# Performance work log

Hardware: AMD Instinct MI355X
Metric: run time of the kernel (lower is better)

The kernel has to match this reference:

```python
import jax, jax.numpy as jnp
import numpy as np

SEGMENT_LENGTHS = (2048, 4096, 8192)
DILATION_RATES = (1, 2, 4)


def _attention(q, k, v):
    # q,k,v: (B, s, h, d); xformers default scale = 1/sqrt(d), no mask, no dropout
    d = q.shape[-1]
    scale = 1.0 / jnp.sqrt(jnp.asarray(d, q.dtype))
    scores = jnp.einsum('bshd,bthd->bhst', q, k) * scale
    p = jax.nn.softmax(scores, axis=-1)
    return jnp.einsum('bhst,bthd->bshd', p, v)


def setup_inputs() -> dict:
    key = jax.random.key(0)
    kq, kk, kv = jax.random.split(key, 3)
    shape = (2, 8192, 12, 64)
    return {
        'query': jax.random.normal(kq, shape, dtype=jnp.float32),
        'key': jax.random.normal(kk, shape, dtype=jnp.float32),
        'value': jax.random.normal(kv, shape, dtype=jnp.float32),
    }


def reference(query, key, value):
    b, n, h, d = query.shape
    num_groups = len(DILATION_RATES)
    group_sizes = [h // num_groups] * num_groups
    for i in range(h % num_groups):
        group_sizes[i] += 1
    out = jnp.zeros_like(query)
    for i, (g, r, s) in enumerate(zip(group_sizes, DILATION_RATES, SEGMENT_LENGTHS)):
        nseg = n // s
        offset = i % r
        hmin, hmax = i * g, (i + 1) * g
        # gather: segment, dilate (stride r), select head group
        qg = query.reshape(b, nseg, s, h, d)[:, :, offset::r, hmin:hmax, :]
        kg = key.reshape(b, nseg, s, h, d)[:, :, offset::r, hmin:hmax, :]
        vg = value.reshape(b, nseg, s, h, d)[:, :, offset::r, hmin:hmax, :]
        sd = qg.shape[2]  # dilated segment length
        x = _attention(
            qg.reshape(b * nseg, sd, g, d),
            kg.reshape(b * nseg, sd, g, d),
            vg.reshape(b * nseg, sd, g, d),
        ).reshape(b, nseg, sd, g, d)
        # normalization over (segments, dilated positions), as in the original
        x = x / x.sum(axis=(1, 2), keepdims=True)
        out_r = out.reshape(b, nseg, s, h, d)
        out_r = out_r.at[:, :, offset::r, hmin:hmax, :].add(x)
        out = out_r.reshape(b, n, h, d)
    return out / num_groups
```

## Files before the change

kernel.cpp:

```cpp
#include <hip/hip_runtime.h>
#include <math.h>

#define TOK_STRIDE 768

typedef __attribute__((ext_vector_type(8))) _Float16 f16x8;
typedef __attribute__((ext_vector_type(16))) float f32x16;

__device__ __forceinline__ int inst_index(int g, int b, int seg, int gh) {
    if (g == 0) return b * 16 + seg * 4 + gh;
    if (g == 1) return 32 + b * 8 + seg * 4 + gh;
    return 48 + b * 4 + gh;
}

__device__ __forceinline__ void decode_inst(int inst, int& g, int& b, int& seg, int& gh) {
    if (inst < 32)      { g = 0; int x = inst;      b = x >> 4; seg = (x >> 2) & 3; gh = x & 3; }
    else if (inst < 48) { g = 1; int x = inst - 32; b = x >> 3; seg = (x >> 2) & 1; gh = x & 3; }
    else                { g = 2; int x = inst - 48; b = x >> 2; seg = 0;            gh = x & 3; }
}

__device__ __forceinline__ long inst_base(int g, int b, int seg, int gh, long& tstep) {
    int r = 1 << g, s = 2048 << g, off = (g == 0) ? 0 : g, h = g * 4 + gh;
    tstep = (long)r * TOK_STRIDE;
    long tok0 = (long)seg * s + off;
    return ((long)b * 8192 + tok0) * TOK_STRIDE + (long)h * 64;
}

__device__ __forceinline__ void h_split(float x, unsigned short& hi, unsigned short& lo) {
    _Float16 h = (_Float16)x;
    _Float16 l = (_Float16)(x - (float)h);
    hi = __builtin_bit_cast(unsigned short, h);
    lo = __builtin_bit_cast(unsigned short, l);
}

__device__ __forceinline__ unsigned h2_rn(float a, float b) {
    unsigned short ua = __builtin_bit_cast(unsigned short, (_Float16)a);
    unsigned short ub = __builtin_bit_cast(unsigned short, (_Float16)b);
    return (unsigned)ua | ((unsigned)ub << 16);
}

__device__ __forceinline__ void gload_lds16(void* lds, const void* g) {
    __builtin_amdgcn_global_load_lds(
        (const __attribute__((address_space(1))) unsigned int*)g,
        (__attribute__((address_space(3))) unsigned int*)lds, 16, 0, 0);
}

__global__ __launch_bounds__(256) void prep_kernel(
    const float* __restrict__ K, const float* __restrict__ V,
    unsigned short* __restrict__ Kh, unsigned short* __restrict__ Kl,
    unsigned short* __restrict__ Vth, unsigned short* __restrict__ Vtl)
{
    const int kt = blockIdx.x, inst = blockIdx.y;
    int g, b, seg, gh; decode_inst(inst, g, b, seg, gh);
    long tstep; const long base = inst_base(g, b, seg, gh, tstep);
    const float* kb = K + base;
    const float* vb = V + base;
    const int t = threadIdx.x;

    __shared__ float Vs[64][72];

    #pragma unroll
    for (int p = 0; p < 4; ++p) {
        int flat = p * 256 + t;
        int key = flat >> 4;
        int d0 = (flat & 15) * 4;
        const long src = ((long)(kt * 64 + key)) * tstep + d0;
        float4 xk = *(const float4*)(kb + src);
        float kvals[4] = {xk.x, xk.y, xk.z, xk.w};
        unsigned short hi[4], lo[4];
        #pragma unroll
        for (int e = 0; e < 4; ++e) h_split(kvals[e], hi[e], lo[e]);
        int dc = d0 >> 4, hh = (d0 >> 3) & 1, j = d0 & 7;
        long idx = ((((long)inst * 32 + kt) * 8 + dc * 2 + hh) * 64 + key) * 8 + j;
        *(ushort4*)(Kh + idx) = make_ushort4(hi[0], hi[1], hi[2], hi[3]);
        *(ushort4*)(Kl + idx) = make_ushort4(lo[0], lo[1], lo[2], lo[3]);
        float4 xv = *(const float4*)(vb + src);
        float vvals[4] = {xv.x, xv.y, xv.z, xv.w};
        #pragma unroll
        for (int e = 0; e < 4; ++e) {
            int d = d0 + e;
            Vs[d][key ^ ((((d) >> 2) & 7) << 3)] = vvals[e];
        }
    }
    __syncthreads();
    #pragma unroll
    for (int p = 0; p < 4; ++p) {
        int flat = p * 256 + t;
        int d = flat >> 4;
        int k40 = (flat & 15) * 4;
        int swz = ((d >> 2) & 7) << 3;
        float4 xv = *(const float4*)&Vs[d][k40 ^ swz];
        float vvals[4] = {xv.x, xv.y, xv.z, xv.w};
        unsigned short hi[4], lo[4];
        #pragma unroll
        for (int e = 0; e < 4; ++e) h_split(vvals[e], hi[e], lo[e]);
        int k = kt * 64 + k40;
        int kc = k >> 4, hh = (k >> 3) & 1, j = k & 7;
        long idx = ((((long)inst * 128 + kc) * 2 + hh) * 64 + d) * 8 + j;
        *(ushort4*)(Vth + idx) = make_ushort4(hi[0], hi[1], hi[2], hi[3]);
        *(ushort4*)(Vtl + idx) = make_ushort4(lo[0], lo[1], lo[2], lo[3]);
    }
}

__global__ __launch_bounds__(256, 2) void attn_kernel(
    const float* __restrict__ Q,
    const unsigned short* __restrict__ Kh, const unsigned short* __restrict__ Kl,
    const unsigned short* __restrict__ Vth, const unsigned short* __restrict__ Vtl,
    float* __restrict__ O)
{
    const int rt = blockIdx.x, inst = blockIdx.y;
    int g, b, seg, gh; decode_inst(inst, g, b, seg, gh);
    long tstep; const long base = inst_base(g, b, seg, gh, tstep);
    const float* qb = Q + base;

    __shared__ unsigned short KVb[2][16384];
    __shared__ unsigned short Pb[4][2048];

    const int t = threadIdx.x;
    const int lane = t & 63;
    const int w = t >> 6;
    const int l31 = lane & 31;
    const int h = lane >> 5;

    const float* qp = qb + (long)(rt * 128 + w * 32 + l31) * tstep;
    f16x8 Qhf[4], Qlf[4];
    #pragma unroll
    for (int dc = 0; dc < 4; ++dc) {
        float4 f0 = *(const float4*)(qp + dc * 16 + h * 8);
        float4 f1 = *(const float4*)(qp + dc * 16 + h * 8 + 4);
        float vals[8] = {f0.x, f0.y, f0.z, f0.w, f1.x, f1.y, f1.z, f1.w};
        #pragma unroll
        for (int j = 0; j < 8; ++j) {
            float x = vals[j] * 0.125f;
            _Float16 hi = (_Float16)x;
            _Float16 lo = (_Float16)(x - (float)hi);
            Qhf[dc][j] = hi;
            Qlf[dc][j] = lo;
        }
    }

    const unsigned short* sbase = (w == 0) ? Kh : (w == 1) ? Kl : (w == 2) ? Vth : Vtl;
    const unsigned short* sp0 = sbase + (long)inst * 131072;
    #pragma unroll
    for (int i = 0; i < 8; ++i)
        gload_lds16(&KVb[0][w * 4096 + i * 512], sp0 + i * 512 + lane * 8);

    f32x16 o0, o1;
    #pragma unroll
    for (int rr = 0; rr < 16; ++rr) { o0[rr] = 0.f; o1[rr] = 0.f; }
    float m = -INFINITY, lsum = 0.f;

    __syncthreads();

    for (int kt = 0; kt < 32; ++kt) {
        const int cb = kt & 1;
        if (kt + 1 < 32) {
            const unsigned short* sp = sp0 + (long)(kt + 1) * 4096;
            #pragma unroll
            for (int i = 0; i < 8; ++i)
                gload_lds16(&KVb[cb ^ 1][w * 4096 + i * 512], sp + i * 512 + lane * 8);
        }

        f32x16 sS[2];
        #pragma unroll
        for (int a = 0; a < 2; ++a)
            #pragma unroll
            for (int rr = 0; rr < 16; ++rr) sS[a][rr] = 0.f;

        #pragma unroll
        for (int dc = 0; dc < 4; ++dc) {
            #pragma unroll
            for (int kt2 = 0; kt2 < 2; ++kt2) {
                int aoff = ((dc * 2 + h) * 64 + kt2 * 32 + l31) * 8;
                f16x8 kh = *(const f16x8*)&KVb[cb][aoff];
                f16x8 kl = *(const f16x8*)&KVb[cb][4096 + aoff];
                sS[kt2] = __builtin_amdgcn_mfma_f32_32x32x16_f16(kh, Qhf[dc], sS[kt2], 0, 0, 0);
                sS[kt2] = __builtin_amdgcn_mfma_f32_32x32x16_f16(kh, Qlf[dc], sS[kt2], 0, 0, 0);
                sS[kt2] = __builtin_amdgcn_mfma_f32_32x32x16_f16(kl, Qhf[dc], sS[kt2], 0, 0, 0);
            }
        }

        float pmax = -INFINITY;
        #pragma unroll
        for (int a = 0; a < 2; ++a)
            #pragma unroll
            for (int rr = 0; rr < 16; ++rr) pmax = fmaxf(pmax, sS[a][rr]);
        pmax = fmaxf(pmax, __shfl_xor(pmax, 32));

        if (!__all(pmax <= m + 8.f)) {
            float mnew = fmaxf(m, pmax);
            float f = __expf(m - mnew);
            m = mnew;
            lsum *= f;
            #pragma unroll
            for (int rr = 0; rr < 16; ++rr) { o0[rr] *= f; o1[rr] *= f; }
        }
        float psum = 0.f;
        #pragma unroll
        for (int a = 0; a < 2; ++a)
            #pragma unroll
            for (int rr = 0; rr < 16; ++rr) {
                float p = __expf(sS[a][rr] - m);
                sS[a][rr] = p;
                psum += p;
            }
        psum += __shfl_xor(psum, 32);
        lsum += psum;

        #pragma unroll
        for (int kt2 = 0; kt2 < 2; ++kt2) {
            #pragma unroll
            for (int qd = 0; qd < 4; ++qd) {
                unsigned w0 = h2_rn(sS[kt2][qd * 4 + 0], sS[kt2][qd * 4 + 1]);
                unsigned w1 = h2_rn(sS[kt2][qd * 4 + 2], sS[kt2][qd * 4 + 3]);
                int k = kt2 * 32 + qd * 8 + 4 * h;
                int kc = k >> 4, hh = (k >> 3) & 1, j = k & 7;
                int idx = ((kc * 2 + hh) * 32 + l31) * 8 + j;
                *(uint2*)&Pb[w][idx] = make_uint2(w0, w1);
            }
        }

        #pragma unroll
        for (int kc = 0; kc < 4; ++kc) {
            f16x8 pf = *(const f16x8*)&Pb[w][((kc * 2 + h) * 32 + l31) * 8];
            int voff = ((kc * 2 + h) * 64 + l31) * 8;
            f16x8 vh0 = *(const f16x8*)&KVb[cb][8192 + voff];
            f16x8 vl0 = *(const f16x8*)&KVb[cb][12288 + voff];
            f16x8 vh1 = *(const f16x8*)&KVb[cb][8192 + voff + 256];
            f16x8 vl1 = *(const f16x8*)&KVb[cb][12288 + voff + 256];
            o0 = __builtin_amdgcn_mfma_f32_32x32x16_f16(vh0, pf, o0, 0, 0, 0);
            o0 = __builtin_amdgcn_mfma_f32_32x32x16_f16(vl0, pf, o0, 0, 0, 0);
            o1 = __builtin_amdgcn_mfma_f32_32x32x16_f16(vh1, pf, o1, 0, 0, 0);
            o1 = __builtin_amdgcn_mfma_f32_32x32x16_f16(vl1, pf, o1, 0, 0, 0);
        }

        __syncthreads();
    }

    float inv = 1.0f / lsum;
    const int q = rt * 128 + w * 32 + l31;
    float* op = O + ((long)inst * 2048 + q) * 64;
    #pragma unroll
    for (int c = 0; c < 4; ++c) {
        int d0 = c * 8 + 4 * h;
        *(float4*)(op + d0) = make_float4(o0[c * 4] * inv, o0[c * 4 + 1] * inv,
                                          o0[c * 4 + 2] * inv, o0[c * 4 + 3] * inv);
        *(float4*)(op + 32 + d0) = make_float4(o1[c * 4] * inv, o1[c * 4 + 1] * inv,
                                               o1[c * 4 + 2] * inv, o1[c * 4 + 3] * inv);
    }
}

__global__ __launch_bounds__(256) void sum_kernel(
    const float* __restrict__ O, double* __restrict__ partial)
{
    const int blk = blockIdx.x;
    const int c   = blockIdx.y;
    const int g   = blk >> 3;
    const int b   = (blk >> 2) & 1;
    const int gh  = blk & 3;
    const int nseg = 4 >> g;
    const int R = nseg << 11;
    const int chunk = R >> 4;

    const int t  = threadIdx.x;
    const int d  = t & 63;
    const int rc = t >> 6;

    double acc = 0.0;
    for (int jr = c * chunk + rc; jr < (c + 1) * chunk; jr += 4) {
        int seg  = jr >> 11;
        int j    = jr & 2047;
        int inst = inst_index(g, b, seg, gh);
        acc += (double)O[(long)inst * 131072 + (long)j * 64 + d];
    }
    __shared__ double red[256];
    red[t] = acc;
    __syncthreads();
    if (rc == 0)
        partial[((long)blk * 16 + c) * 64 + d] =
            red[d] + red[64 + d] + red[128 + d] + red[192 + d];
}

__global__ void inv_kernel(const double* __restrict__ partial, double* __restrict__ invden)
{
    const int blk = blockIdx.x;
    const int d   = threadIdx.x;
    double s = 0.0;
    #pragma unroll
    for (int c = 0; c < 16; ++c) s += partial[((long)blk * 16 + c) * 64 + d];
    invden[blk * 64 + d] = 1.0 / (3.0 * s);
}

__global__ __launch_bounds__(256) void out_kernel(
    const float* __restrict__ O, const double* __restrict__ invden,
    float* __restrict__ out)
{
    const int f = blockIdx.x * 256 + threadIdx.x;
    const int d  = f & 63;
    const int hh = (f >> 6) % 12;
    const int tk = (f / 768) % 8192;
    const int b  = f / (768 * 8192);

    const int g  = hh >> 2;
    const int gh = hh & 3;
    const int r  = 1 << g;
    const int off = (g == 0) ? 0 : g;

    const int seg = tk >> (11 + g);
    const int pos = tk - (seg << (11 + g));
    const int rem = pos - off;

    float val = 0.f;
    if (rem >= 0 && (rem & (r - 1)) == 0) {
        const int j = rem >> g;
        const int inst = inst_index(g, b, seg, gh);
        float num = O[(long)inst * 131072 + (long)j * 64 + d];
        double iv = invden[(long)(g * 8 + b * 4 + gh) * 64 + d];
        val = (float)((double)num * iv);
    }
    out[f] = val;
}

extern "C" void kernel_launch(void* const* d_in, const int* in_sizes, int n_in,
                              void* d_out, int out_size, void* d_ws, size_t ws_size,
                              hipStream_t stream) {
    const float* q = (const float*)d_in[0];
    const float* k = (const float*)d_in[1];
    const float* v = (const float*)d_in[2];
    float* out = (float*)d_out;

    char* ws = (char*)d_ws;
    double* invden  = (double*)(ws);
    double* partial = (double*)(ws + 12288);
    float*  Ows     = (float*)(ws + 208896);
    unsigned short* Khp  = (unsigned short*)(ws + 29569024);
    unsigned short* Klp  = (unsigned short*)(ws + 44249088);
    unsigned short* Vthp = (unsigned short*)(ws + 58929152);
    unsigned short* Vtlp = (unsigned short*)(ws + 73609216);

    dim3 gprep(32, 56);
    prep_kernel<<<gprep, 256, 0, stream>>>(k, v, Khp, Klp, Vthp, Vtlp);
    dim3 gattn(16, 56);
    attn_kernel<<<gattn, 256, 0, stream>>>(q, Khp, Klp, Vthp, Vtlp, Ows);
    dim3 gsum(24, 16);
    sum_kernel<<<gsum, 256, 0, stream>>>(Ows, partial);
    inv_kernel<<<24, 64, 0, stream>>>(partial, invden);
    out_kernel<<<49152, 256, 0, stream>>>(Ows, invden, out);
}
```

Before: 406.3 us.

## Restructure attention LDS pipeline: single V buffer, register P shuffle, 3 blocks/CU

The attention kernel now keeps only K double-buffered and V in a single buffer loaded at the start of each iteration, with a partial vmcnt wait and a barrier before PV. The P tile is passed to the PV MFMAs through lane shuffles instead of a round trip through LDS. Together these shrink the LDS footprint so occupancy can rise to 3 blocks per CU, and s_setprio is set around the MFMA phases. The grid is flattened to interleave instances, and prep_kernel is widened to 8 elements per thread with 16-byte stores. The risk is that V loads become less hidden, and the hand-written waitcnt adds fragility.

```diff
diff --git a/kernel.cpp b/kernel.cpp
--- a/kernel.cpp
+++ b/kernel.cpp
@@ -5,6 +5,7 @@
 
 typedef __attribute__((ext_vector_type(8))) _Float16 f16x8;
 typedef __attribute__((ext_vector_type(16))) float f32x16;
+typedef __attribute__((ext_vector_type(4))) unsigned uint4v;
 
 __device__ __forceinline__ int inst_index(int g, int b, int seg, int gh) {
     if (g == 0) return b * 16 + seg * 4 + gh;
@@ -42,6 +43,21 @@
     __builtin_amdgcn_global_load_lds(
         (const __attribute__((address_space(1))) unsigned int*)g,
         (__attribute__((address_space(3))) unsigned int*)lds, 16, 0, 0);
+}
+
+__device__ __forceinline__ uint4v split8(float4 a, float4 b, uint4v& lo4) {
+    float v[8] = {a.x, a.y, a.z, a.w, b.x, b.y, b.z, b.w};
+    unsigned short hi[8], lo[8];
+    #pragma unroll
+    for (int e = 0; e < 8; ++e) h_split(v[e], hi[e], lo[e]);
+    uint4v h4, l4;
+    #pragma unroll
+    for (int wdi = 0; wdi < 4; ++wdi) {
+        h4[wdi] = (unsigned)hi[2 * wdi] | ((unsigned)hi[2 * wdi + 1] << 16);
+        l4[wdi] = (unsigned)lo[2 * wdi] | ((unsigned)lo[2 * wdi + 1] << 16);
+    }
+    lo4 = l4;
+    return h4;
 }
 
 __global__ __launch_bounds__(256) void prep_kernel(
@@ -59,61 +75,57 @@
     __shared__ float Vs[64][72];
 
     #pragma unroll
-    for (int p = 0; p < 4; ++p) {
-        int flat = p * 256 + t;
-        int key = flat >> 4;
-        int d0 = (flat & 15) * 4;
-        const long src = ((long)(kt * 64 + key)) * tstep + d0;
-        float4 xk = *(const float4*)(kb + src);
-        float kvals[4] = {xk.x, xk.y, xk.z, xk.w};
-        unsigned short hi[4], lo[4];
-        #pragma unroll
-        for (int e = 0; e < 4; ++e) h_split(kvals[e], hi[e], lo[e]);
-        int dc = d0 >> 4, hh = (d0 >> 3) & 1, j = d0 & 7;
-        long idx = ((((long)inst * 32 + kt) * 8 + dc * 2 + hh) * 64 + key) * 8 + j;
-        *(ushort4*)(Kh + idx) = make_ushort4(hi[0], hi[1], hi[2], hi[3]);
-        *(ushort4*)(Kl + idx) = make_ushort4(lo[0], lo[1], lo[2], lo[3]);
-        float4 xv = *(const float4*)(vb + src);
-        float vvals[4] = {xv.x, xv.y, xv.z, xv.w};
-        #pragma unroll
-        for (int e = 0; e < 4; ++e) {
+    for (int p = 0; p < 2; ++p) {
+        int item = p * 256 + t;
+        int key = item >> 3, dg = item & 7, d0 = dg * 8;
+        long src = (long)(kt * 64 + key) * tstep + d0;
+        float4 ka  = *(const float4*)(kb + src);
+        float4 ka2 = *(const float4*)(kb + src + 4);
+        uint4v lo4;
+        uint4v hi4 = split8(ka, ka2, lo4);
+        long idx = ((((long)inst * 32 + kt) * 8 + dg) * 64 + key) * 8;
+        *(uint4v*)(Kh + idx) = hi4;
+        *(uint4v*)(Kl + idx) = lo4;
+        float4 va  = *(const float4*)(vb + src);
+        float4 va2 = *(const float4*)(vb + src + 4);
+        float vv[8] = {va.x, va.y, va.z, va.w, va2.x, va2.y, va2.z, va2.w};
+        #pragma unroll
+        for (int e = 0; e < 8; ++e) {
             int d = d0 + e;
-            Vs[d][key ^ ((((d) >> 2) & 7) << 3)] = vvals[e];
+            Vs[d][key ^ (((d >> 2) & 7) << 3)] = vv[e];
         }
     }
     __syncthreads();
     #pragma unroll
-    for (int p = 0; p < 4; ++p) {
-        int flat = p * 256 + t;
-        int d = flat >> 4;
-        int k40 = (flat & 15) * 4;
+    for (int p = 0; p < 2; ++p) {
+        int item = p * 256 + t;
+        int d = item >> 3, kg = item & 7, k0 = kg * 8;
         int swz = ((d >> 2) & 7) << 3;
-        float4 xv = *(const float4*)&Vs[d][k40 ^ swz];
-        float vvals[4] = {xv.x, xv.y, xv.z, xv.w};
-        unsigned short hi[4], lo[4];
-        #pragma unroll
-        for (int e = 0; e < 4; ++e) h_split(vvals[e], hi[e], lo[e]);
-        int k = kt * 64 + k40;
-        int kc = k >> 4, hh = (k >> 3) & 1, j = k & 7;
-        long idx = ((((long)inst * 128 + kc) * 2 + hh) * 64 + d) * 8 + j;
-        *(ushort4*)(Vth + idx) = make_ushort4(hi[0], hi[1], hi[2], hi[3]);
-        *(ushort4*)(Vtl + idx) = make_ushort4(lo[0], lo[1], lo[2], lo[3]);
-    }
-}
-
-__global__ __launch_bounds__(256, 2) void attn_kernel(
+        float4 x0 = *(const float4*)&Vs[d][k0 ^ swz];
+        float4 x1 = *(const float4*)&Vs[d][(k0 + 4) ^ swz];
+        uint4v lo4;
+        uint4v hi4 = split8(x0, x1, lo4);
+        long idx = ((((long)inst * 128 + kt * 4 + (kg >> 1)) * 2 + (kg & 1)) * 64 + d) * 8;
+        *(uint4v*)(Vth + idx) = hi4;
+        *(uint4v*)(Vtl + idx) = lo4;
+    }
+}
+
+__global__ __launch_bounds__(256, 3) void attn_kernel(
     const float* __restrict__ Q,
     const unsigned short* __restrict__ Kh, const unsigned short* __restrict__ Kl,
     const unsigned short* __restrict__ Vth, const unsigned short* __restrict__ Vtl,
     float* __restrict__ O)
 {
-    const int rt = blockIdx.x, inst = blockIdx.y;
+    const int bx = blockIdx.x;
+    const int inst = bx % 56;
+    const int rt   = bx / 56;
     int g, b, seg, gh; decode_inst(inst, g, b, seg, gh);
     long tstep; const long base = inst_base(g, b, seg, gh, tstep);
     const float* qb = Q + base;
 
-    __shared__ unsigned short KVb[2][16384];
-    __shared__ unsigned short Pb[4][2048];
+    __shared__ unsigned short Kb[2][8192];
+    __shared__ unsigned short Vb[8192];
 
     const int t = threadIdx.x;
     const int lane = t & 63;
@@ -138,11 +150,18 @@
         }
     }
 
-    const unsigned short* sbase = (w == 0) ? Kh : (w == 1) ? Kl : (w == 2) ? Vth : Vtl;
-    const unsigned short* sp0 = sbase + (long)inst * 131072;
-    #pragma unroll
-    for (int i = 0; i < 8; ++i)
-        gload_lds16(&KVb[0][w * 4096 + i * 512], sp0 + i * 512 + lane * 8);
+    const unsigned short* KsA = Kh  + (long)inst * 131072;
+    const unsigned short* KsB = Kl  + (long)inst * 131072;
+    const unsigned short* VsA = Vth + (long)inst * 131072;
+    const unsigned short* VsB = Vtl + (long)inst * 131072;
+    const int s0 = w * 4;
+
+    #pragma unroll
+    for (int i = 0; i < 4; ++i) {
+        int s = s0 + i;
+        const unsigned short* src = ((s < 8) ? KsA : KsB) + (s & 7) * 512 + lane * 8;
+        gload_lds16(&Kb[0][s * 512], src);
+    }
 
     f32x16 o0, o1;
     #pragma unroll
@@ -151,14 +170,26 @@
 
     __syncthreads();
 
+    #pragma unroll 1
     for (int kt = 0; kt < 32; ++kt) {
         const int cb = kt & 1;
+
+        #pragma unroll
+        for (int i = 0; i < 4; ++i) {
+            int s = s0 + i;
+            const unsigned short* src = ((s < 8) ? VsA : VsB) + (long)kt * 4096 + (s & 7) * 512 + lane * 8;
+            gload_lds16(&Vb[s * 512], src);
+        }
+        asm volatile("" ::: "memory");
         if (kt + 1 < 32) {
-            const unsigned short* sp = sp0 + (long)(kt + 1) * 4096;
-            #pragma unroll
-            for (int i = 0; i < 8; ++i)
-                gload_lds16(&KVb[cb ^ 1][w * 4096 + i * 512], sp + i * 512 + lane * 8);
-        }
+            #pragma unroll
+            for (int i = 0; i < 4; ++i) {
+                int s = s0 + i;
+                const unsigned short* src = ((s < 8) ? KsA : KsB) + (long)(kt + 1) * 4096 + (s & 7) * 512 + lane * 8;
+                gload_lds16(&Kb[cb ^ 1][s * 512], src);
+            }
+        }
+        asm volatile("" ::: "memory");
 
         f32x16 sS[2];
         #pragma unroll
@@ -166,18 +197,20 @@
             #pragma unroll
             for (int rr = 0; rr < 16; ++rr) sS[a][rr] = 0.f;
 
+        __builtin_amdgcn_s_setprio(1);
         #pragma unroll
         for (int dc = 0; dc < 4; ++dc) {
             #pragma unroll
             for (int kt2 = 0; kt2 < 2; ++kt2) {
                 int aoff = ((dc * 2 + h) * 64 + kt2 * 32 + l31) * 8;
-                f16x8 kh = *(const f16x8*)&KVb[cb][aoff];
-                f16x8 kl = *(const f16x8*)&KVb[cb][4096 + aoff];
+                f16x8 kh = *(const f16x8*)&Kb[cb][aoff];
+                f16x8 kl = *(const f16x8*)&Kb[cb][4096 + aoff];
                 sS[kt2] = __builtin_amdgcn_mfma_f32_32x32x16_f16(kh, Qhf[dc], sS[kt2], 0, 0, 0);
                 sS[kt2] = __builtin_amdgcn_mfma_f32_32x32x16_f16(kh, Qlf[dc], sS[kt2], 0, 0, 0);
                 sS[kt2] = __builtin_amdgcn_mfma_f32_32x32x16_f16(kl, Qhf[dc], sS[kt2], 0, 0, 0);
             }
         }
+        __builtin_amdgcn_s_setprio(0);
 
         float pmax = -INFINITY;
         #pragma unroll
@@ -206,32 +239,45 @@
         psum += __shfl_xor(psum, 32);
         lsum += psum;
 
-        #pragma unroll
-        for (int kt2 = 0; kt2 < 2; ++kt2) {
+        unsigned pw[2][4][2];
+        #pragma unroll
+        for (int kt2 = 0; kt2 < 2; ++kt2)
             #pragma unroll
             for (int qd = 0; qd < 4; ++qd) {
-                unsigned w0 = h2_rn(sS[kt2][qd * 4 + 0], sS[kt2][qd * 4 + 1]);
-                unsigned w1 = h2_rn(sS[kt2][qd * 4 + 2], sS[kt2][qd * 4 + 3]);
-                int k = kt2 * 32 + qd * 8 + 4 * h;
-                int kc = k >> 4, hh = (k >> 3) & 1, j = k & 7;
-                int idx = ((kc * 2 + hh) * 32 + l31) * 8 + j;
-                *(uint2*)&Pb[w][idx] = make_uint2(w0, w1);
+                pw[kt2][qd][0] = h2_rn(sS[kt2][qd * 4 + 0], sS[kt2][qd * 4 + 1]);
+                pw[kt2][qd][1] = h2_rn(sS[kt2][qd * 4 + 2], sS[kt2][qd * 4 + 3]);
             }
-        }
-
+
+        if (kt + 1 < 32) { asm volatile("s_waitcnt vmcnt(4)" ::: "memory"); }
+        else             { asm volatile("s_waitcnt vmcnt(0)" ::: "memory"); }
+        __builtin_amdgcn_s_barrier();
+        asm volatile("" ::: "memory");
+
+        __builtin_amdgcn_s_setprio(1);
         #pragma unroll
         for (int kc = 0; kc < 4; ++kc) {
-            f16x8 pf = *(const f16x8*)&Pb[w][((kc * 2 + h) * 32 + l31) * 8];
+            const int kt2 = kc >> 1, q0 = (kc & 1) * 2;
+            unsigned a0 = pw[kt2][q0][0],     a1 = pw[kt2][q0][1];
+            unsigned b0 = pw[kt2][q0 + 1][0], b1 = pw[kt2][q0 + 1][1];
+            unsigned oa0 = __shfl_xor(a0, 32), oa1 = __shfl_xor(a1, 32);
+            unsigned ob0 = __shfl_xor(b0, 32), ob1 = __shfl_xor(b1, 32);
+            uint4v u;
+            u[0] = h ? ob0 : a0;
+            u[1] = h ? ob1 : a1;
+            u[2] = h ? b0  : oa0;
+            u[3] = h ? b1  : oa1;
+            f16x8 pf = __builtin_bit_cast(f16x8, u);
             int voff = ((kc * 2 + h) * 64 + l31) * 8;
-            f16x8 vh0 = *(const f16x8*)&KVb[cb][8192 + voff];
-            f16x8 vl0 = *(const f16x8*)&KVb[cb][12288 + voff];
-            f16x8 vh1 = *(const f16x8*)&KVb[cb][8192 + voff + 256];
-            f16x8 vl1 = *(const f16x8*)&KVb[cb][12288 + voff + 256];
+            f16x8 vh0 = *(const f16x8*)&Vb[voff];
+            f16x8 vl0 = *(const f16x8*)&Vb[4096 + voff];
+            f16x8 vh1 = *(const f16x8*)&Vb[voff + 256];
+            f16x8 vl1 = *(const f16x8*)&Vb[4096 + voff + 256];
             o0 = __builtin_amdgcn_mfma_f32_32x32x16_f16(vh0, pf, o0, 0, 0, 0);
             o0 = __builtin_amdgcn_mfma_f32_32x32x16_f16(vl0, pf, o0, 0, 0, 0);
             o1 = __builtin_amdgcn_mfma_f32_32x32x16_f16(vh1, pf, o1, 0, 0, 0);
             o1 = __builtin_amdgcn_mfma_f32_32x32x16_f16(vl1, pf, o1, 0, 0, 0);
         }
+        __builtin_amdgcn_s_setprio(0);
 
         __syncthreads();
     }
@@ -339,8 +385,7 @@
 
     dim3 gprep(32, 56);
     prep_kernel<<<gprep, 256, 0, stream>>>(k, v, Khp, Klp, Vthp, Vtlp);
-    dim3 gattn(16, 56);
-    attn_kernel<<<gattn, 256, 0, stream>>>(q, Khp, Klp, Vthp, Vtlp, Ows);
+    attn_kernel<<<896, 256, 0, stream>>>(q, Khp, Klp, Vthp, Vtlp, Ows);
     dim3 gsum(24, 16);
     sum_kernel<<<gsum, 256, 0, stream>>>(Ows, partial);
     inv_kernel<<<24, 64, 0, stream>>>(partial, invden);
```

New measurement: 398.1 us. 1.02x faster.
